# Kernel tuning notes

Hardware: AMD Instinct MI355X
Metric: run time of the kernel (lower is better)

Reference implementation:

```python
import jax, jax.numpy as jnp
import numpy as np

B, T, N, PREV_DIM, CURR_DIM = 8, 32, 500, 200, 128
HEADS, UNITS, MSG_UNITS = 4, 64, 64


def setup_inputs() -> dict:
    key = jax.random.key(0)
    k = jax.random.split(key, 6)
    prev_features = jax.random.normal(k[0], (B, N, PREV_DIM), jnp.float32)
    curr_hidden = jax.random.normal(k[1], (B, T, N, CURR_DIM), jnp.float32)
    # glorot-ish small params
    W_src = jax.random.normal(k[2], (HEADS, PREV_DIM, UNITS), jnp.float32) * 0.05
    W_dst = jax.random.normal(k[3], (HEADS, PREV_DIM, UNITS), jnp.float32) * 0.05
    a = jax.random.normal(k[4], (HEADS, UNITS, 1), jnp.float32) * 0.1
    W_msg = jax.random.normal(k[5], (HEADS, CURR_DIM, MSG_UNITS), jnp.float32) * 0.05
    return {"prev_features": prev_features, "curr_hidden": curr_hidden,
            "W_src": W_src, "W_dst": W_dst, "a": a, "W_msg": W_msg}


def reference(prev_features, curr_hidden, W_src, W_dst, a, W_msg):
    # prev_features: [B, N, Dp]; curr_hidden: [B, T, N, Dc]
    heads = W_src.shape[0]
    head_outputs = []
    for h in range(heads):  # small fixed loop over heads (as in original)
        h_src = jnp.einsum('bnd,du->bnu', prev_features, W_src[h])  # [B,N,U]
        h_dst = jnp.einsum('bnd,du->bnu', prev_features, W_dst[h])  # [B,N,U]
        # GATv2 additive scoring: lrelu(src_i + dst_j) . a   -> [B,N,N]
        pairwise = jax.nn.leaky_relu(h_src[:, :, None, :] + h_dst[:, None, :, :], 0.2)
        scores = jnp.einsum('bnmu,u->bnm', pairwise, a[h, :, 0])
        attn = jax.nn.softmax(scores, axis=-1)  # [B,N,N]; dropout is identity at inference
        msg = jnp.einsum('btnd,du->btnu', curr_hidden, W_msg[h])  # [B,T,N,Mu]
        # same graph applied at every timestep (tf.repeat + batched matmul)
        h_prime = jnp.einsum('bnm,btmu->btnu', attn, msg)  # [B,T,N,Mu]
        head_outputs.append(h_prime)
    return jnp.mean(jnp.stack(head_outputs, axis=-1), axis=-1)
```

## Files before the change

kernel.cpp:

```cpp
#include <hip/hip_runtime.h>

#define B_ 8
#define T_ 32
#define N_ 500
#define DP 200
#define DC 128
#define H_ 4
#define U_ 64
#define NP 512
#define COLS (T_ * U_)
#define K4 (H_ * NP)

typedef __attribute__((ext_vector_type(8))) short bf16x8;
typedef __attribute__((ext_vector_type(4))) float f32x4;
typedef __attribute__((ext_vector_type(2))) float f32x2;

typedef const __attribute__((address_space(1))) void* gcptr_t;
typedef __attribute__((address_space(3))) void* lptr_t;

__device__ __forceinline__ void async16(const void* g, void* lds) {
    __builtin_amdgcn_global_load_lds((gcptr_t)g, (lptr_t)lds, 16, 0, 0);
}

__device__ __forceinline__ ushort f2bf(float f) {
    unsigned u = __float_as_uint(f);
    unsigned r = (u + 0x7FFFu + ((u >> 16) & 1u)) >> 16;
    return (ushort)r;
}

__device__ __forceinline__ f32x2 pk_add_sv(unsigned long long sp, f32x2 dp) {
    f32x2 t;
    asm("v_pk_add_f32 %0, %1, %2" : "=v"(t) : "s"(sp), "v"(dp));
    return t;
}

#define MFMA __builtin_amdgcn_mfma_f32_16x16x32_bf16

__global__ void __launch_bounds__(512) proj_all2(
    const float* __restrict__ prev, const float* __restrict__ Wsrc,
    const float* __restrict__ Wdst, const float* __restrict__ a_all,
    const float* __restrict__ Wmsg, float* __restrict__ hsrc,
    float* __restrict__ hdst, float* __restrict__ qv, ushort* __restrict__ WT)
{
    __shared__ float rows[8 * DP];
    const int tid = threadIdx.x;
    const int bn0 = blockIdx.x * 8;

    if (blockIdx.x < 128 && tid < 256) {
        int idx = blockIdx.x * 256 + tid;
        int h = idx >> 13, u = (idx >> 7) & 63, d = idx & 127;
        WT[idx] = f2bf(0.25f * Wmsg[((size_t)h * DC + d) * U_ + u]);
    }

    for (int e = tid; e < 8 * DP; e += 512) rows[e] = prev[(size_t)bn0 * DP + e];
    __syncthreads();
    const int u = tid & 63;
    const int h = (tid >> 6) & 3;
    const int isdst = tid >> 8;
    const float* W = (isdst ? Wdst : Wsrc) + (size_t)h * DP * U_;
    float acc[8] = {};
#pragma unroll 4
    for (int d = 0; d < DP; ++d) {
        float w = W[d * U_ + u];
#pragma unroll
        for (int r = 0; r < 8; ++r)
            acc[r] = fmaf(rows[r * DP + d], w, acc[r]);
    }
    float* o = isdst ? hdst : hsrc;
#pragma unroll
    for (int r = 0; r < 8; ++r) {
        int bn = bn0 + r, b = bn / N_, n = bn - b * N_;
        o[(((size_t)b * H_ + h) * N_ + n) * U_ + u] = acc[r];
    }
    if (isdst) {
        const int lane = tid & 63;
        const float av = a_all[(size_t)h * U_ + lane];
#pragma unroll
        for (int r = 0; r < 8; ++r) {
            float v = acc[r] * av;
            for (int off = 1; off < 64; off <<= 1) v += __shfl_xor(v, off);
            if (lane == 0) {
                int bn = bn0 + r, b = bn / N_, n = bn - b * N_;
                qv[((size_t)b * H_ + h) * NP + n] = v;
            }
        }
    }
}

__global__ void __launch_bounds__(512) attn_softmax9(
    const float* __restrict__ hsrc, const float* __restrict__ hdst,
    const float* __restrict__ a_all, const float* __restrict__ qv,
    ushort* __restrict__ attnB)
{
    const int i0 = blockIdx.x * 8, b = blockIdx.y, h = blockIdx.z;
    const int tid = threadIdx.x;
    __shared__ float red[8 * 8];
    __shared__ float s_mx[8], s_rs[8];

    const float* ap = a_all + (size_t)h * U_;
    const float* hb = hsrc + (((size_t)b * H_ + h) * N_) * U_;
    const unsigned long long* sr8[8];
#pragma unroll
    for (int r = 0; r < 8; ++r)
        sr8[r] = (const unsigned long long*)
            (hb + (size_t)min(i0 + r, N_ - 1) * U_);

    const int j = tid;
    const bool valid = j < N_;
    const float4* dp =
        (const float4*)&hdst[(((size_t)b * H_ + h) * N_ + (valid ? j : 0)) * U_];
    const float qj = qv[((size_t)b * H_ + h) * NP + j];

    float av[8] = {0.f, 0.f, 0.f, 0.f, 0.f, 0.f, 0.f, 0.f};
#pragma unroll 1
    for (int kc = 0; kc < 8; ++kc) {
        const int o = kc * 8;
        float4 A = dp[kc * 2 + 0];
        float4 Bv = dp[kc * 2 + 1];
        f32x2 dvp[4];
        dvp[0] = (f32x2){A.x, A.y};  dvp[1] = (f32x2){A.z, A.w};
        dvp[2] = (f32x2){Bv.x, Bv.y}; dvp[3] = (f32x2){Bv.z, Bv.w};
#pragma unroll
        for (int p = 0; p < 4; ++p) {
            const float a_lo = ap[o + p * 2];
            const float a_hi = ap[o + p * 2 + 1];
#pragma unroll
            for (int r = 0; r < 8; ++r) {
                f32x2 t = pk_add_sv(sr8[r][kc * 4 + p], dvp[p]);
                av[r] = fmaf(fabsf(t.x), a_lo, av[r]);
                av[r] = fmaf(fabsf(t.y), a_hi, av[r]);
            }
        }
    }
    const float q6 = 0.6f * qj;
    float sc[8];
#pragma unroll
    for (int r = 0; r < 8; ++r)
        sc[r] = valid ? fmaf(0.4f, av[r], q6) : -1e30f;

    const int wave = tid >> 6, lane = tid & 63;
#pragma unroll
    for (int r = 0; r < 8; ++r) {
        float m = sc[r];
        for (int off = 1; off < 64; off <<= 1) m = fmaxf(m, __shfl_xor(m, off));
        if (lane == 0) red[wave * 8 + r] = m;
    }
    __syncthreads();
    if (tid < 8) {
        float mm = red[tid];
        for (int w = 1; w < 8; ++w) mm = fmaxf(mm, red[w * 8 + tid]);
        s_mx[tid] = mm;
    }
    __syncthreads();
    float e[8];
#pragma unroll
    for (int r = 0; r < 8; ++r) {
        e[r] = __expf(sc[r] - s_mx[r]);
        float s = e[r];
        for (int off = 1; off < 64; off <<= 1) s += __shfl_xor(s, off);
        if (lane == 0) red[wave * 8 + r] = s;
    }
    __syncthreads();
    if (tid < 8) {
        float ss = 0.f;
        for (int w = 0; w < 8; ++w) ss += red[w * 8 + tid];
        s_rs[tid] = 1.0f / ss;
    }
    __syncthreads();
#pragma unroll
    for (int r = 0; r < 8; ++r)
        attnB[(((size_t)b * H_ + h) * NP + i0 + r) * NP + j] =
            f2bf(e[r] * s_rs[r]);
}

__global__ void __launch_bounds__(512) msg_all(
    const float* __restrict__ curr, const ushort* __restrict__ WT,
    ushort* __restrict__ msgT)
{
    __shared__ ushort st[64 * 128];
    const int tid = threadIdx.x;
    const int m0 = blockIdx.x * 128, t = blockIdx.y, b = blockIdx.z;
    const int wave = tid >> 6, lane = tid & 63;
    const int r15 = lane & 15, quad = lane >> 4;
    const int wrow = (wave >> 1) * 32;
    const int wu = wave & 1;

    const float* cbase = curr + (size_t)(b * T_ + t) * N_ * DC;

    bf16x8 af[2][4];
#pragma unroll
    for (int f = 0; f < 2; ++f) {
        const int gm = min(m0 + wrow + f * 16 + r15, N_ - 1);
        const float* rp = cbase + (size_t)gm * DC + quad * 8;
#pragma unroll
        for (int ks = 0; ks < 4; ++ks) {
            float4 lo = *(const float4*)&rp[ks * 32];
            float4 hi = *(const float4*)&rp[ks * 32 + 4];
            bf16x8 v;
            v[0] = (short)f2bf(lo.x); v[1] = (short)f2bf(lo.y);
            v[2] = (short)f2bf(lo.z); v[3] = (short)f2bf(lo.w);
            v[4] = (short)f2bf(hi.x); v[5] = (short)f2bf(hi.y);
            v[6] = (short)f2bf(hi.z); v[7] = (short)f2bf(hi.w);
            af[f][ks] = v;
        }
    }

    const ushort* wbase = WT + (size_t)(wu * 32 + r15) * DC + quad * 8;

    const int rrow = tid >> 3, rseg = tid & 7;

#pragma unroll 1
    for (int h = 0; h < H_; ++h) {
        const ushort* wh = wbase + (size_t)h * U_ * DC;
        f32x4 acc[2][2] = {};
#pragma unroll
        for (int ks = 0; ks < 4; ++ks) {
            bf16x8 bg[2];
#pragma unroll
            for (int g = 0; g < 2; ++g)
                bg[g] = *(const bf16x8*)&wh[(size_t)(g * 16) * DC + ks * 32];
#pragma unroll
            for (int f = 0; f < 2; ++f)
#pragma unroll
                for (int g = 0; g < 2; ++g)
                    acc[f][g] = MFMA(af[f][ks], bg[g], acc[f][g], 0, 0, 0);
        }
        if (h) __syncthreads();
#pragma unroll
        for (int f = 0; f < 2; ++f)
#pragma unroll
            for (int g = 0; g < 2; ++g) {
                const int u = wu * 32 + g * 16 + r15;
                const int mp = wrow + f * 16 + quad * 4;
                const int c = (mp >> 2) ^ (u & 7);
                ushort4 o;
                o.x = f2bf(acc[f][g][0]); o.y = f2bf(acc[f][g][1]);
                o.z = f2bf(acc[f][g][2]); o.w = f2bf(acc[f][g][3]);
                *(ushort4*)&st[u * 128 + c * 4] = o;
            }
        __syncthreads();
        unsigned long long ch[4];
#pragma unroll
        for (int k = 0; k < 4; ++k) {
            const int c = (rseg * 4 + k) ^ (rrow & 7);
            ch[k] = *(const unsigned long long*)&st[rrow * 128 + c * 4];
        }
        ushort* gp = &msgT[(((size_t)b * H_ + h) * COLS + t * U_ + rrow) * NP
                           + m0 + rseg * 16];
        ((unsigned long long*)gp)[0] = ch[0];
        ((unsigned long long*)gp)[1] = ch[1];
        ((unsigned long long*)gp)[2] = ch[2];
        ((unsigned long long*)gp)[3] = ch[3];
    }
}

__global__ void __launch_bounds__(512) gemm_big3(
    const ushort* __restrict__ msgT, const ushort* __restrict__ attnB,
    float* __restrict__ out)
{
    __shared__ ushort As[128 * 64];
    __shared__ ushort Bs[128 * 64];
    const int tid = threadIdx.x;
    const int mt = blockIdx.x, nt = blockIdx.y, b = blockIdx.z;

    const int wave = tid >> 6, lane = tid & 63;
    const int r15 = lane & 15, quad = lane >> 4;
    const int wm = wave >> 2, wn = wave & 3;
    const int lrow = lane >> 3, lch = lane & 7;

    f32x4 acc[4][2] = {};
    for (int kk = 0; kk < K4; kk += 64) {
        const int hh = kk >> 9, ko = kk & (NP - 1);
        const ushort* Ab = msgT + (((size_t)b * H_ + hh) * COLS + mt * 128) * NP + ko;
        const ushort* Bb = attnB + (((size_t)b * H_ + hh) * NP + nt * 128) * NP + ko;
#pragma unroll
        for (int l = 0; l < 2; ++l) {
            const int R0 = wave * 16 + l * 8;
            const int row = R0 + lrow;
            const int gch = lch ^ (row & 7);
            async16(Ab + (size_t)row * NP + gch * 8, &As[R0 * 64]);
            async16(Bb + (size_t)row * NP + gch * 8, &Bs[R0 * 64]);
        }
        __syncthreads();
#pragma unroll
        for (int ks = 0; ks < 2; ++ks) {
            bf16x8 af[4], bg[2];
#pragma unroll
            for (int f = 0; f < 4; ++f) {
                int row = wm * 64 + f * 16 + r15;
                int c = (ks * 4 + quad) ^ (row & 7);
                af[f] = *(const bf16x8*)&As[row * 64 + c * 8];
            }
#pragma unroll
            for (int g = 0; g < 2; ++g) {
                int row = wn * 32 + g * 16 + r15;
                int c = (ks * 4 + quad) ^ (row & 7);
                bg[g] = *(const bf16x8*)&Bs[row * 64 + c * 8];
            }
#pragma unroll
            for (int f = 0; f < 4; ++f)
#pragma unroll
                for (int g = 0; g < 2; ++g)
                    acc[f][g] = MFMA(af[f], bg[g], acc[f][g], 0, 0, 0);
        }
        __syncthreads();
    }

    const int t = mt * 2 + wm;
#pragma unroll
    for (int f = 0; f < 4; ++f)
#pragma unroll
        for (int g = 0; g < 2; ++g) {
            int u = f * 16 + quad * 4;
            int i = nt * 128 + wn * 32 + g * 16 + r15;
            if (i < N_) {
                float4 v;
                v.x = acc[f][g][0]; v.y = acc[f][g][1];
                v.z = acc[f][g][2]; v.w = acc[f][g][3];
                *(float4*)&out[(((size_t)b * T_ + t) * N_ + i) * U_ + u] = v;
            }
        }
}

__global__ void __launch_bounds__(256) msg_mfma(
    const float* __restrict__ curr, const ushort* __restrict__ WTh,
    ushort* __restrict__ msgT)
{
    __shared__ ushort As[128 * 136];
    __shared__ ushort Bs[64 * 136];
    const int tid = threadIdx.x;
    const int m0 = blockIdx.x * 128, t = blockIdx.y, b = blockIdx.z;

    const float* cbase = curr + (size_t)(b * T_ + t) * N_ * DC;
#pragma unroll
    for (int it = 0; it < 16; ++it) {
        int e = it * 1024 + tid * 4;
        int r = e >> 7, c = e & 127;
        int gm = m0 + r;
        float4 v; v.x = v.y = v.z = v.w = 0.f;
        if (gm < N_) v = *(const float4*)&cbase[(size_t)gm * DC + c];
        ushort4 o;
        o.x = f2bf(v.x); o.y = f2bf(v.y); o.z = f2bf(v.z); o.w = f2bf(v.w);
        *(ushort4*)&As[r * 136 + c] = o;
    }
#pragma unroll
    for (int it = 0; it < 4; ++it) {
        int e = it * 2048 + tid * 8;
        int u = e >> 7, d = e & 127;
        *(uint4*)&Bs[u * 136 + d] = *(const uint4*)&WTh[u * 128 + d];
    }
    __syncthreads();

    const int wave = tid >> 6, lane = tid & 63;
    const int r15 = lane & 15, quad = lane >> 4;
    const int wm = wave >> 1, wu = wave & 1;

    f32x4 acc[4][2] = {};
#pragma unroll
    for (int ks = 0; ks < 4; ++ks) {
        bf16x8 af[4], bg[2];
#pragma unroll
        for (int f = 0; f < 4; ++f)
            af[f] = *(const bf16x8*)&As[(wm * 64 + f * 16 + r15) * 136 + ks * 32 + quad * 8];
#pragma unroll
        for (int g = 0; g < 2; ++g)
            bg[g] = *(const bf16x8*)&Bs[(wu * 32 + g * 16 + r15) * 136 + ks * 32 + quad * 8];
#pragma unroll
        for (int f = 0; f < 4; ++f)
#pragma unroll
            for (int g = 0; g < 2; ++g)
                acc[f][g] = MFMA(af[f], bg[g], acc[f][g], 0, 0, 0);
    }
#pragma unroll
    for (int f = 0; f < 4; ++f)
#pragma unroll
        for (int g = 0; g < 2; ++g) {
            int m = m0 + wm * 64 + f * 16 + quad * 4;
            int u = wu * 32 + g * 16 + r15;
            int col = t * U_ + u;
            ushort4 o;
            o.x = f2bf(acc[f][g][0]); o.y = f2bf(acc[f][g][1]);
            o.z = f2bf(acc[f][g][2]); o.w = f2bf(acc[f][g][3]);
            *(ushort4*)&msgT[((size_t)b * COLS + col) * NP + m] = o;
        }
}

__global__ void __launch_bounds__(256) gemm_mfma(
    const ushort* __restrict__ msgT, const ushort* __restrict__ attnB,
    float* __restrict__ out, int h, int init)
{
    __shared__ ushort As[64 * 72];
    __shared__ ushort Bs[64 * 72];
    const int tid = threadIdx.x;
    const int ct = blockIdx.x, it = blockIdx.y, b = blockIdx.z;

    const ushort* Ab = msgT + ((size_t)b * COLS + ct * 64) * NP;
    const ushort* Bb = attnB + (((size_t)b * H_ + h) * NP + it * 64) * NP;

    const int wave = tid >> 6, lane = tid & 63;
    const int r15 = lane & 15, quad = lane >> 4;
    const int wm = wave >> 1, wn = wave & 1;
    const int srow = tid >> 3, scol = (tid & 7) * 8;

    f32x4 acc[2][2] = {};
    for (int kk = 0; kk < NP; kk += 64) {
#pragma unroll
        for (int it2 = 0; it2 < 2; ++it2) {
            int rr = it2 * 32 + srow;
            *(uint4*)&As[rr * 72 + scol] = *(const uint4*)&Ab[(size_t)rr * NP + kk + scol];
            *(uint4*)&Bs[rr * 72 + scol] = *(const uint4*)&Bb[(size_t)rr * NP + kk + scol];
        }
        __syncthreads();
#pragma unroll
        for (int ks = 0; ks < 2; ++ks) {
            bf16x8 af[2], bg[2];
#pragma unroll
            for (int f = 0; f < 2; ++f)
                af[f] = *(const bf16x8*)&As[(wm * 32 + f * 16 + r15) * 72 + ks * 32 + quad * 8];
#pragma unroll
            for (int g = 0; g < 2; ++g)
                bg[g] = *(const bf16x8*)&Bs[(wn * 32 + g * 16 + r15) * 72 + ks * 32 + quad * 8];
#pragma unroll
            for (int f = 0; f < 2; ++f)
#pragma unroll
                for (int g = 0; g < 2; ++g)
                    acc[f][g] = MFMA(af[f], bg[g], acc[f][g], 0, 0, 0);
        }
        __syncthreads();
    }

    const int t = ct;
#pragma unroll
    for (int f = 0; f < 2; ++f)
#pragma unroll
        for (int g = 0; g < 2; ++g) {
            int u = wm * 32 + f * 16 + quad * 4;
            int i = it * 64 + wn * 32 + g * 16 + r15;
            if (i < N_) {
                float* op = out + (((size_t)b * T_ + t) * N_ + i) * U_ + u;
                float4 v;
                v.x = acc[f][g][0]; v.y = acc[f][g][1];
                v.z = acc[f][g][2]; v.w = acc[f][g][3];
                if (!init) {
                    float4 old = *(const float4*)op;
                    v.x += old.x; v.y += old.y; v.z += old.z; v.w += old.w;
                }
                *(float4*)op = v;
            }
        }
}

extern "C" void kernel_launch(void* const* d_in, const int* in_sizes, int n_in,
                              void* d_out, int out_size, void* d_ws, size_t ws_size,
                              hipStream_t stream)
{
    const float* prev = (const float*)d_in[0];
    const float* curr = (const float*)d_in[1];
    const float* Wsrc = (const float*)d_in[2];
    const float* Wdst = (const float*)d_in[3];
    const float* avec = (const float*)d_in[4];
    const float* Wmsg = (const float*)d_in[5];
    float* out = (float*)d_out;

    const size_t attnB_b = (size_t)B_ * H_ * NP * NP * 2;
    const size_t msgT4_b = (size_t)B_ * H_ * COLS * NP * 2;
    const size_t msgT1_b = (size_t)B_ * COLS * NP * 2;
    const size_t WT_b    = (size_t)H_ * U_ * DC * 2;
    const size_t hx_b    = (size_t)B_ * H_ * N_ * U_ * 4;
    const size_t qv_b    = (size_t)B_ * H_ * NP * 4;

    const bool fused = ws_size >= attnB_b + msgT4_b + WT_b + 2 * hx_b + qv_b;
    const size_t msg_b = fused ? msgT4_b : msgT1_b;

    ushort* attnB = (ushort*)d_ws;
    ushort* msgT  = (ushort*)((char*)d_ws + attnB_b);
    ushort* WT    = (ushort*)((char*)d_ws + attnB_b + msg_b);
    float*  hsrc  = (float*)((char*)WT + WT_b);
    float*  hdst  = (float*)((char*)hsrc + hx_b);
    float*  qv    = (float*)((char*)hdst + hx_b);

    proj_all2<<<500, 512, 0, stream>>>(prev, Wsrc, Wdst, avec, Wmsg,
                                       hsrc, hdst, qv, WT);
    attn_softmax9<<<dim3(64, B_, H_), 512, 0, stream>>>(hsrc, hdst, avec, qv, attnB);

    if (fused) {
        msg_all<<<dim3(4, T_, B_), 512, 0, stream>>>(curr, WT, msgT);
        gemm_big3<<<dim3(16, 4, B_), 512, 0, stream>>>(msgT, attnB, out);
    } else {
        for (int h = 0; h < H_; ++h) {
            msg_mfma<<<dim3(4, T_, B_), 256, 0, stream>>>(
                curr, WT + (size_t)h * U_ * DC, msgT);
            gemm_mfma<<<dim3(32, 8, B_), 256, 0, stream>>>(
                msgT, attnB, out, h, h == 0 ? 1 : 0);
        }
    }
}
```

Measured before the change: 266.2 us.

## Merge attention softmax and message projection into one interleaved kernel launch

Combines the attention-softmax kernel and the message-projection kernel into a single launch of 3072 blocks. Blocks are interleaved by index modulo 3: two of every three compute softmax rows and one computes a message tile. The goal is to overlap the ALU-bound scoring work with the memory- and MFMA-bound message projection, and to remove one launch boundary. The cost is a shared LDS allocation sized for the larger branch and a divergent per-block branch. The unfused fallback path keeps the separate kernels.

```diff
diff --git a/kernel.cpp b/kernel.cpp
--- a/kernel.cpp
+++ b/kernel.cpp
@@ -87,6 +87,177 @@
     }
 }
 
+__global__ void __launch_bounds__(512) phase2(
+    const float* __restrict__ hsrc, const float* __restrict__ hdst,
+    const float* __restrict__ a_all, const float* __restrict__ qv,
+    ushort* __restrict__ attnB,
+    const float* __restrict__ curr, const ushort* __restrict__ WT,
+    ushort* __restrict__ msgT)
+{
+    __shared__ char sh[64 * 128 * 2];
+    const int bid = blockIdx.x;
+    const int tid = threadIdx.x;
+    const int sel = bid % 3;
+
+    if (sel == 2) {
+        ushort* st = (ushort*)sh;
+        const int midx = bid / 3;
+        const int m0 = (midx & 3) * 128, t = (midx >> 2) & 31, b = midx >> 7;
+        const int wave = tid >> 6, lane = tid & 63;
+        const int r15 = lane & 15, quad = lane >> 4;
+        const int wrow = (wave >> 1) * 32;
+        const int wu = wave & 1;
+
+        const float* cbase = curr + (size_t)(b * T_ + t) * N_ * DC;
+
+        bf16x8 af[2][4];
+#pragma unroll
+        for (int f = 0; f < 2; ++f) {
+            const int gm = min(m0 + wrow + f * 16 + r15, N_ - 1);
+            const float* rp = cbase + (size_t)gm * DC + quad * 8;
+#pragma unroll
+            for (int ks = 0; ks < 4; ++ks) {
+                float4 lo = *(const float4*)&rp[ks * 32];
+                float4 hi = *(const float4*)&rp[ks * 32 + 4];
+                bf16x8 v;
+                v[0] = (short)f2bf(lo.x); v[1] = (short)f2bf(lo.y);
+                v[2] = (short)f2bf(lo.z); v[3] = (short)f2bf(lo.w);
+                v[4] = (short)f2bf(hi.x); v[5] = (short)f2bf(hi.y);
+                v[6] = (short)f2bf(hi.z); v[7] = (short)f2bf(hi.w);
+                af[f][ks] = v;
+            }
+        }
+
+        const ushort* wbase = WT + (size_t)(wu * 32 + r15) * DC + quad * 8;
+        const int rrow = tid >> 3, rseg = tid & 7;
+
+#pragma unroll 1
+        for (int h = 0; h < H_; ++h) {
+            const ushort* wh = wbase + (size_t)h * U_ * DC;
+            f32x4 acc[2][2] = {};
+#pragma unroll
+            for (int ks = 0; ks < 4; ++ks) {
+                bf16x8 bg[2];
+#pragma unroll
+                for (int g = 0; g < 2; ++g)
+                    bg[g] = *(const bf16x8*)&wh[(size_t)(g * 16) * DC + ks * 32];
+#pragma unroll
+                for (int f = 0; f < 2; ++f)
+#pragma unroll
+                    for (int g = 0; g < 2; ++g)
+                        acc[f][g] = MFMA(af[f][ks], bg[g], acc[f][g], 0, 0, 0);
+            }
+            if (h) __syncthreads();
+#pragma unroll
+            for (int f = 0; f < 2; ++f)
+#pragma unroll
+                for (int g = 0; g < 2; ++g) {
+                    const int u = wu * 32 + g * 16 + r15;
+                    const int mp = wrow + f * 16 + quad * 4;
+                    const int c = (mp >> 2) ^ (u & 7);
+                    ushort4 o;
+                    o.x = f2bf(acc[f][g][0]); o.y = f2bf(acc[f][g][1]);
+                    o.z = f2bf(acc[f][g][2]); o.w = f2bf(acc[f][g][3]);
+                    *(ushort4*)&st[u * 128 + c * 4] = o;
+                }
+            __syncthreads();
+            unsigned long long ch[4];
+#pragma unroll
+            for (int k = 0; k < 4; ++k) {
+                const int c = (rseg * 4 + k) ^ (rrow & 7);
+                ch[k] = *(const unsigned long long*)&st[rrow * 128 + c * 4];
+            }
+            ushort* gp = &msgT[(((size_t)b * H_ + h) * COLS + t * U_ + rrow) * NP
+                               + m0 + rseg * 16];
+            ((unsigned long long*)gp)[0] = ch[0];
+            ((unsigned long long*)gp)[1] = ch[1];
+            ((unsigned long long*)gp)[2] = ch[2];
+            ((unsigned long long*)gp)[3] = ch[3];
+        }
+    } else {
+        float* red  = (float*)sh;
+        float* s_mx = red + 64;
+        float* s_rs = s_mx + 8;
+        const int aidx = (bid / 3) * 2 + sel;
+        const int i0 = (aidx & 63) * 8, b = (aidx >> 6) & 7, h = aidx >> 9;
+
+        const float* ap = a_all + (size_t)h * U_;
+        const float* hb = hsrc + (((size_t)b * H_ + h) * N_) * U_;
+        const unsigned long long* sr8[8];
+#pragma unroll
+        for (int r = 0; r < 8; ++r)
+            sr8[r] = (const unsigned long long*)
+                (hb + (size_t)min(i0 + r, N_ - 1) * U_);
+
+        const int j = tid;
+        const bool valid = j < N_;
+        const float4* dp =
+            (const float4*)&hdst[(((size_t)b * H_ + h) * N_ + (valid ? j : 0)) * U_];
+        const float qj = qv[((size_t)b * H_ + h) * NP + j];
+
+        float av[8] = {0.f, 0.f, 0.f, 0.f, 0.f, 0.f, 0.f, 0.f};
+#pragma unroll 1
+        for (int kc = 0; kc < 8; ++kc) {
+            float4 A = dp[kc * 2 + 0];
+            float4 Bv = dp[kc * 2 + 1];
+            f32x2 dvp[4];
+            dvp[0] = (f32x2){A.x, A.y};  dvp[1] = (f32x2){A.z, A.w};
+            dvp[2] = (f32x2){Bv.x, Bv.y}; dvp[3] = (f32x2){Bv.z, Bv.w};
+            const int o = kc * 8;
+#pragma unroll
+            for (int p = 0; p < 4; ++p) {
+                const float a_lo = ap[o + p * 2];
+                const float a_hi = ap[o + p * 2 + 1];
+#pragma unroll
+                for (int r = 0; r < 8; ++r) {
+                    f32x2 t2 = pk_add_sv(sr8[r][kc * 4 + p], dvp[p]);
+                    av[r] = fmaf(fabsf(t2.x), a_lo, av[r]);
+                    av[r] = fmaf(fabsf(t2.y), a_hi, av[r]);
+                }
+            }
+        }
+        const float q6 = 0.6f * qj;
+        float sc[8];
+#pragma unroll
+        for (int r = 0; r < 8; ++r)
+            sc[r] = valid ? fmaf(0.4f, av[r], q6) : -1e30f;
+
+        const int wave = tid >> 6, lane = tid & 63;
+#pragma unroll
+        for (int r = 0; r < 8; ++r) {
+            float m = sc[r];
+            for (int off = 1; off < 64; off <<= 1) m = fmaxf(m, __shfl_xor(m, off));
+            if (lane == 0) red[wave * 8 + r] = m;
+        }
+        __syncthreads();
+        if (tid < 8) {
+            float mm = red[tid];
+            for (int w = 1; w < 8; ++w) mm = fmaxf(mm, red[w * 8 + tid]);
+            s_mx[tid] = mm;
+        }
+        __syncthreads();
+        float e[8];
+#pragma unroll
+        for (int r = 0; r < 8; ++r) {
+            e[r] = __expf(sc[r] - s_mx[r]);
+            float s = e[r];
+            for (int off = 1; off < 64; off <<= 1) s += __shfl_xor(s, off);
+            if (lane == 0) red[wave * 8 + r] = s;
+        }
+        __syncthreads();
+        if (tid < 8) {
+            float ss = 0.f;
+            for (int w = 0; w < 8; ++w) ss += red[w * 8 + tid];
+            s_rs[tid] = 1.0f / ss;
+        }
+        __syncthreads();
+#pragma unroll
+        for (int r = 0; r < 8; ++r)
+            attnB[(((size_t)b * H_ + h) * NP + i0 + r) * NP + j] =
+                f2bf(e[r] * s_rs[r]);
+    }
+}
+
 __global__ void __launch_bounds__(512) attn_softmax9(
     const float* __restrict__ hsrc, const float* __restrict__ hdst,
     const float* __restrict__ a_all, const float* __restrict__ qv,
@@ -171,87 +342,6 @@
     for (int r = 0; r < 8; ++r)
         attnB[(((size_t)b * H_ + h) * NP + i0 + r) * NP + j] =
             f2bf(e[r] * s_rs[r]);
-}
-
-__global__ void __launch_bounds__(512) msg_all(
-    const float* __restrict__ curr, const ushort* __restrict__ WT,
-    ushort* __restrict__ msgT)
-{
-    __shared__ ushort st[64 * 128];
-    const int tid = threadIdx.x;
-    const int m0 = blockIdx.x * 128, t = blockIdx.y, b = blockIdx.z;
-    const int wave = tid >> 6, lane = tid & 63;
-    const int r15 = lane & 15, quad = lane >> 4;
-    const int wrow = (wave >> 1) * 32;
-    const int wu = wave & 1;
-
-    const float* cbase = curr + (size_t)(b * T_ + t) * N_ * DC;
-
-    bf16x8 af[2][4];
-#pragma unroll
-    for (int f = 0; f < 2; ++f) {
-        const int gm = min(m0 + wrow + f * 16 + r15, N_ - 1);
-        const float* rp = cbase + (size_t)gm * DC + quad * 8;
-#pragma unroll
-        for (int ks = 0; ks < 4; ++ks) {
-            float4 lo = *(const float4*)&rp[ks * 32];
-            float4 hi = *(const float4*)&rp[ks * 32 + 4];
-            bf16x8 v;
-            v[0] = (short)f2bf(lo.x); v[1] = (short)f2bf(lo.y);
-            v[2] = (short)f2bf(lo.z); v[3] = (short)f2bf(lo.w);
-            v[4] = (short)f2bf(hi.x); v[5] = (short)f2bf(hi.y);
-            v[6] = (short)f2bf(hi.z); v[7] = (short)f2bf(hi.w);
-            af[f][ks] = v;
-        }
-    }
-
-    const ushort* wbase = WT + (size_t)(wu * 32 + r15) * DC + quad * 8;
-
-    const int rrow = tid >> 3, rseg = tid & 7;
-
-#pragma unroll 1
-    for (int h = 0; h < H_; ++h) {
-        const ushort* wh = wbase + (size_t)h * U_ * DC;
-        f32x4 acc[2][2] = {};
-#pragma unroll
-        for (int ks = 0; ks < 4; ++ks) {
-            bf16x8 bg[2];
-#pragma unroll
-            for (int g = 0; g < 2; ++g)
-                bg[g] = *(const bf16x8*)&wh[(size_t)(g * 16) * DC + ks * 32];
-#pragma unroll
-            for (int f = 0; f < 2; ++f)
-#pragma unroll
-                for (int g = 0; g < 2; ++g)
-                    acc[f][g] = MFMA(af[f][ks], bg[g], acc[f][g], 0, 0, 0);
-        }
-        if (h) __syncthreads();
-#pragma unroll
-        for (int f = 0; f < 2; ++f)
-#pragma unroll
-            for (int g = 0; g < 2; ++g) {
-                const int u = wu * 32 + g * 16 + r15;
-                const int mp = wrow + f * 16 + quad * 4;
-                const int c = (mp >> 2) ^ (u & 7);
-                ushort4 o;
-                o.x = f2bf(acc[f][g][0]); o.y = f2bf(acc[f][g][1]);
-                o.z = f2bf(acc[f][g][2]); o.w = f2bf(acc[f][g][3]);
-                *(ushort4*)&st[u * 128 + c * 4] = o;
-            }
-        __syncthreads();
-        unsigned long long ch[4];
-#pragma unroll
-        for (int k = 0; k < 4; ++k) {
-            const int c = (rseg * 4 + k) ^ (rrow & 7);
-            ch[k] = *(const unsigned long long*)&st[rrow * 128 + c * 4];
-        }
-        ushort* gp = &msgT[(((size_t)b * H_ + h) * COLS + t * U_ + rrow) * NP
-                           + m0 + rseg * 16];
-        ((unsigned long long*)gp)[0] = ch[0];
-        ((unsigned long long*)gp)[1] = ch[1];
-        ((unsigned long long*)gp)[2] = ch[2];
-        ((unsigned long long*)gp)[3] = ch[3];
-    }
 }
 
 __global__ void __launch_bounds__(512) gemm_big3(
@@ -481,12 +571,13 @@
 
     proj_all2<<<500, 512, 0, stream>>>(prev, Wsrc, Wdst, avec, Wmsg,
                                        hsrc, hdst, qv, WT);
-    attn_softmax9<<<dim3(64, B_, H_), 512, 0, stream>>>(hsrc, hdst, avec, qv, attnB);
 
     if (fused) {
-        msg_all<<<dim3(4, T_, B_), 512, 0, stream>>>(curr, WT, msgT);
+        phase2<<<3072, 512, 0, stream>>>(hsrc, hdst, avec, qv, attnB,
+                                         curr, WT, msgT);
         gemm_big3<<<dim3(16, 4, B_), 512, 0, stream>>>(msgT, attnB, out);
     } else {
+        attn_softmax9<<<dim3(64, B_, H_), 512, 0, stream>>>(hsrc, hdst, avec, qv, attnB);
         for (int h = 0; h < H_; ++h) {
             msg_mfma<<<dim3(4, T_, B_), 256, 0, stream>>>(
                 curr, WT + (size_t)h * U_ * DC, msgT);
```

New measurement: 262.2 us. Within noise of the previous version (-1.5%).
